# Kernel optimization log

Hardware: AMD Instinct MI355X
Metric: run time of the kernel (lower is better)

The kernel has to match this reference:

```python
import jax, jax.numpy as jnp
import numpy as np

MAX_FRAMES = 12
TOPK = 49
NUM_SAMPLES = 500
SIGMA = 0.05
EPS = 1e-5
NOISE_KEY = jax.random.key(1)


def _ln(x, g, b):
    m = x.mean(-1, keepdims=True)
    v = ((x - m) ** 2).mean(-1, keepdims=True)
    return (x - m) / jnp.sqrt(v + EPS) * g + b


def _gelu(x):
    return jax.nn.gelu(x, approximate=False)  # torch nn.GELU default is exact erf


def _predict(x, guid, ln_in_g, ln_in_b, W_in, ln_gd_g, ln_gd_b, W_gd, W_out1, W_out2):
    # x: (b, N, D), guid: (b, 1, D) -> score (b, N, 1)
    b, N, D = x.shape
    local = _gelu(_ln(x, ln_in_g, ln_in_b) @ W_in)            # (b, N, D/2)
    glob = _gelu(_ln(guid, ln_gd_g, ln_gd_b) @ W_gd)          # (b, 1, D/2); LN is per-token so repeat-then-LN == LN-then-broadcast
    glob = jnp.broadcast_to(glob, (b, N, glob.shape[-1]))
    h = jnp.concatenate([local, glob], axis=-1)               # (b, N, D)
    return jnp.tanh(_gelu(h @ W_out1) @ W_out2)               # (b, N, 1)


def _perturbed_topk(scores):
    # scores: (b, d) -> soft indicators (b, k, d); same math as one_hot(sorted topk idx).mean over samples,
    # computed by scatter-add instead of materializing the (b, ns, k, d) one-hot tensor.
    b, d = scores.shape
    noise = jax.random.normal(NOISE_KEY, (b, NUM_SAMPLES, d), scores.dtype)
    perturbed = scores[:, None, :] + SIGMA * noise            # (b, ns, d)
    _, idx = jax.lax.top_k(perturbed, TOPK)                   # (b, ns, k)
    idx = jnp.sort(idx, axis=-1)
    bi = jnp.arange(b)[:, None, None]
    ki = jnp.arange(TOPK)[None, None, :]
    ind = jnp.zeros((b, TOPK, d), scores.dtype).at[bi, ki, idx].add(1.0 / NUM_SAMPLES)
    return ind


def setup_inputs() -> dict:
    key = jax.random.key(0)
    ks = jax.random.split(key, 9)
    B, F, N, D = 8, MAX_FRAMES, 196, 512
    H = D // 2
    s = 0.02
    return {
        "x": jax.random.normal(ks[0], (B, F * N, D), jnp.float32),
        "guidance_frame": jax.random.normal(ks[1], (B, F, D), jnp.float32),
        "guidance_sentence": jax.random.normal(ks[2], (B, 1, D), jnp.float32),
        "ln_in_g": jnp.ones((D,), jnp.float32),
        "ln_in_b": jnp.zeros((D,), jnp.float32),
        "W_in": jax.random.normal(ks[3], (D, H), jnp.float32) * s,
        "ln_gd_g": jnp.ones((D,), jnp.float32),
        "ln_gd_b": jnp.zeros((D,), jnp.float32),
        "W_gd": jax.random.normal(ks[4], (D, H), jnp.float32) * s,
        "W_out1": jax.random.normal(ks[5], (D, H), jnp.float32) * s,
        "W_out2": jax.random.normal(ks[6], (H, 1), jnp.float32) * s,
    }


def reference(x, guidance_frame, guidance_sentence, ln_in_g, ln_in_b, W_in, ln_gd_g, ln_gd_b, W_gd, W_out1, W_out2):
    B, L, D = x.shape
    N = L // MAX_FRAMES
    xf = x.reshape(B * MAX_FRAMES, N, D)                       # (b', N, D)
    gf = guidance_frame.reshape(B * MAX_FRAMES, 1, D)
    gs = jnp.broadcast_to(guidance_sentence, (B, MAX_FRAMES, D)).reshape(B * MAX_FRAMES, 1, D)
    s1 = _predict(xf, gf, ln_in_g, ln_in_b, W_in, ln_gd_g, ln_gd_b, W_gd, W_out1, W_out2)[..., 0]
    s2 = _predict(xf, gs, ln_in_g, ln_in_b, W_in, ln_gd_g, ln_gd_b, W_gd, W_out1, W_out2)[..., 0]
    score = s1 + s2                                            # (b', N)
    ind = _perturbed_topk(score)                               # (b', k, N)
    selected = jnp.einsum('bkl,bld->bkd', ind, xf)             # (b', k, D)
    return selected.reshape(B, MAX_FRAMES, TOPK, D)
```

## Files before the change

kernel.cpp:

```cpp
#include <hip/hip_runtime.h>
#include <stdint.h>

#define DEV __device__ __forceinline__

#define BP 96
#define NTOK 196
#define DIM 512
#define HID 256
#define NS 500
#define TOPK 49
#define ROWS (BP * NTOK)
#define GBLK (ROWS / 32)
#define SPB 10
#define CNTSZ (TOPK * NTOK)

typedef _Float16 f16x8 __attribute__((ext_vector_type(8)));
typedef float f32x4 __attribute__((ext_vector_type(4)));

DEV float gelu32(float v) {
  return 0.5f * v * (1.0f + erff(v * 0.70710678f));
}

DEV void threefry2x32(uint32_t x0, uint32_t x1, uint32_t& o0, uint32_t& o1) {
  const uint32_t k0 = 0u, k1 = 1u;
  const uint32_t k2 = 0x1BD11BDAu ^ k0 ^ k1;
  x0 += k0; x1 += k1;
#define TF_R(r) { x0 += x1; x1 = (x1 << (r)) | (x1 >> (32 - (r))); x1 ^= x0; }
  TF_R(13) TF_R(15) TF_R(26) TF_R(6)
  x0 += k1; x1 += k2 + 1u;
  TF_R(17) TF_R(29) TF_R(16) TF_R(24)
  x0 += k2; x1 += k0 + 2u;
  TF_R(13) TF_R(15) TF_R(26) TF_R(6)
  x0 += k0; x1 += k1 + 3u;
  TF_R(17) TF_R(29) TF_R(16) TF_R(24)
  x0 += k1; x1 += k2 + 4u;
  TF_R(13) TF_R(15) TF_R(26) TF_R(6)
  x0 += k2; x1 += k0 + 5u;
#undef TF_R
  o0 = x0; o1 = x1;
}

DEV float erfinv_xla(float x) {
  float w = -__logf(fmaf(-x, x, 1.0f));
  float ws = w - 2.5f;
  float ps = 2.81022636e-08f;
  ps = fmaf(ps, ws, 3.43273939e-07f);
  ps = fmaf(ps, ws, -3.5233877e-06f);
  ps = fmaf(ps, ws, -4.39150654e-06f);
  ps = fmaf(ps, ws, 0.00021858087f);
  ps = fmaf(ps, ws, -0.00125372503f);
  ps = fmaf(ps, ws, -0.00417768164f);
  ps = fmaf(ps, ws, 0.246640727f);
  ps = fmaf(ps, ws, 1.50140941f);
  float r = ps;
  if (__ballot(w >= 5.0f) != 0ull) {
    float wl = sqrtf(w) - 3.0f;
    float pl = -0.000200214257f;
    pl = fmaf(pl, wl, 0.000100950558f);
    pl = fmaf(pl, wl, 0.00134934322f);
    pl = fmaf(pl, wl, -0.00367342844f);
    pl = fmaf(pl, wl, 0.00573950773f);
    pl = fmaf(pl, wl, -0.0076224613f);
    pl = fmaf(pl, wl, 0.00943887047f);
    pl = fmaf(pl, wl, 1.00167406f);
    pl = fmaf(pl, wl, 2.83297682f);
    r = (w < 5.0f) ? ps : pl;
  }
  return r * x;
}

DEV float noise_at(unsigned g) {
  unsigned o0, o1;
  threefry2x32(0u, g, o0, o1);
  unsigned bits = o0 ^ o1;
  float f = __uint_as_float((bits >> 9) | 0x3f800000u) - 1.0f;
  float u = f * 2.0f - 0.99999994f;
  u = fmaxf(-0.99999994f, u);
  return 1.41421356f * erfinv_xla(u);
}

DEV size_t pack_idx(int k, int col) {
  int t = k >> 5, kg = (k >> 3) & 3, e = k & 7;
  return (((size_t)(t * 4 + kg) * 256) + col) * 8 + e;
}

#define PRE_GLOB 192
#define PRE_PREP 512
#define PRE_STATS (ROWS / 4)
__global__ __launch_bounds__(256) void k_pre(
    const float* __restrict__ gf, const float* __restrict__ gs,
    const float* __restrict__ lng, const float* __restrict__ lnb,
    const float* __restrict__ Wgd, const float* __restrict__ Wout1,
    float* __restrict__ cout,
    const float* __restrict__ Win,
    const float* __restrict__ g_in, const float* __restrict__ b_in,
    _Float16* __restrict__ Pgh, _Float16* __restrict__ Pgl,
    _Float16* __restrict__ P1h, _Float16* __restrict__ P1l,
    float* __restrict__ gwv, float* __restrict__ bwv,
    const float* __restrict__ x, float* __restrict__ stats) {
  const int bid = blockIdx.x;
  if (bid < PRE_GLOB) {
    int bq = bid >> 1, which = bid & 1;
    const float* row = which ? (gs + (size_t)(bq / 12) * DIM) : (gf + (size_t)bq * DIM);
    __shared__ float lx[DIM];
    __shared__ float sg[HID];
    __shared__ double sred[8];
    int tid = threadIdx.x, lane = tid & 63, wv = tid >> 6;
    float v0 = row[tid], v1 = row[tid + 256];
    double s = (double)v0 + v1, q = (double)v0 * v0 + (double)v1 * v1;
    #pragma unroll
    for (int m = 1; m < 64; m <<= 1) { s += __shfl_xor(s, m); q += __shfl_xor(q, m); }
    if (lane == 0) { sred[wv * 2] = s; sred[wv * 2 + 1] = q; }
    __syncthreads();
    double ts = sred[0] + sred[2] + sred[4] + sred[6];
    double tq = sred[1] + sred[3] + sred[5] + sred[7];
    double mean = ts / 512.0;
    double var = tq / 512.0 - mean * mean;
    float mn = (float)mean;
    float rs = (float)(1.0 / sqrt(var + 1e-5));
    lx[tid]       = (v0 - mn) * rs * lng[tid] + lnb[tid];
    lx[tid + 256] = (v1 - mn) * rs * lng[tid + 256] + lnb[tid + 256];
    __syncthreads();
    float acc = 0.0f;
    for (int d = 0; d < DIM; ++d) acc = fmaf(lx[d], Wgd[(size_t)d * HID + tid], acc);
    sg[tid] = gelu32(acc);
    __syncthreads();
    float c = 0.0f;
    for (int j = 0; j < HID; ++j) c = fmaf(sg[j], Wout1[(size_t)(HID + j) * HID + tid], c);
    cout[((size_t)which * BP + bq) * HID + tid] = c;
  } else if (bid < PRE_GLOB + PRE_PREP) {
    int b2 = bid - PRE_GLOB;
    int n = b2 & 255, half = b2 >> 8;
    if (half == 0) {
      __shared__ float wred[8];
      int tid = threadIdx.x, lane = tid & 63, wv = tid >> 6;
      float sgv = 0.0f, sbv = 0.0f;
      #pragma unroll
      for (int kk = 0; kk < 2; ++kk) {
        int k = tid + kk * 256;
        float w = Win[(size_t)k * HID + n];
        float wg = w * g_in[k];
        _Float16 h = (_Float16)wg;
        size_t pi = pack_idx(k, n);
        Pgh[pi] = h;
        Pgl[pi] = (_Float16)(wg - (float)h);
        sgv += wg;
        sbv = fmaf(b_in[k], w, sbv);
      }
      #pragma unroll
      for (int m = 1; m < 64; m <<= 1) { sgv += __shfl_xor(sgv, m); sbv += __shfl_xor(sbv, m); }
      if (lane == 0) { wred[wv * 2] = sgv; wred[wv * 2 + 1] = sbv; }
      __syncthreads();
      if (tid == 0) {
        gwv[n] = wred[0] + wred[2] + wred[4] + wred[6];
        bwv[n] = wred[1] + wred[3] + wred[5] + wred[7];
      }
    } else {
      int k = threadIdx.x;
      float v = Wout1[(size_t)k * HID + n];
      _Float16 h = (_Float16)v;
      size_t pi = pack_idx(k, n);
      P1h[pi] = h;
      P1l[pi] = (_Float16)(v - (float)h);
    }
  } else {
    int r = (bid - PRE_GLOB - PRE_PREP) * 4 + (threadIdx.x >> 6);
    int lane = threadIdx.x & 63;
    const float4* xr = (const float4*)(x + (size_t)r * DIM);
    float4 a = xr[lane], c = xr[lane + 64];
    double s = (double)a.x + a.y + a.z + a.w + (double)c.x + c.y + c.z + c.w;
    double q = (double)a.x * a.x + (double)a.y * a.y + (double)a.z * a.z + (double)a.w * a.w +
               (double)c.x * c.x + (double)c.y * c.y + (double)c.z * c.z + (double)c.w * c.w;
    #pragma unroll
    for (int m = 1; m < 64; m <<= 1) { s += __shfl_xor(s, m); q += __shfl_xor(q, m); }
    if (lane == 0) {
      double mean = s / 512.0;
      double var = q / 512.0 - mean * mean;
      stats[r * 2]     = (float)mean;
      stats[r * 2 + 1] = (float)(1.0 / sqrt(var + 1e-5));
    }
  }
}

#define LOADA(src0, src1, t, pb)                                               \
  {                                                                            \
    axv[pb][0] = *(const float4*)((src0) + (t) * 32);                          \
    axv[pb][1] = *(const float4*)((src0) + (t) * 32 + 4);                      \
    axv[pb][2] = *(const float4*)((src1) + (t) * 32);                          \
    axv[pb][3] = *(const float4*)((src1) + (t) * 32 + 4);                      \
  }

#define LOADB(bh, bl, t, pb)                                                   \
  {                                                                            \
    _Pragma("unroll")                                                          \
    for (int ni = 0; ni < 4; ++ni) {                                           \
      bxh[pb][ni] = *(const f16x8*)((bh) + (size_t)(t) * 8192 + ni * 128);     \
      bxl[pb][ni] = *(const f16x8*)((bl) + (size_t)(t) * 8192 + ni * 128);     \
    }                                                                          \
  }

#define SPLITA(pb, fah, fal)                                                   \
  {                                                                            \
    _Pragma("unroll")                                                          \
    for (int mi = 0; mi < 2; ++mi) {                                           \
      float va[8];                                                             \
      *(float4*)&va[0] = axv[pb][mi * 2];                                      \
      *(float4*)&va[4] = axv[pb][mi * 2 + 1];                                  \
      _Pragma("unroll")                                                        \
      for (int e = 0; e < 8; ++e) {                                            \
        _Float16 h = (_Float16)va[e];                                          \
        fah[mi][e] = h;                                                        \
        fal[mi][e] = (_Float16)(va[e] - (float)h);                             \
      }                                                                        \
    }                                                                          \
  }

#define MFMA_CHUNK(pb, fah, fal)                                               \
  {                                                                            \
    _Pragma("unroll")                                                          \
    for (int mi = 0; mi < 2; ++mi)                                             \
      _Pragma("unroll")                                                        \
      for (int ni = 0; ni < 4; ++ni) {                                         \
        acc[mi][ni] = __builtin_amdgcn_mfma_f32_16x16x32_f16(fah[mi], bxh[pb][ni], acc[mi][ni], 0, 0, 0); \
        acc[mi][ni] = __builtin_amdgcn_mfma_f32_16x16x32_f16(fah[mi], bxl[pb][ni], acc[mi][ni], 0, 0, 0); \
        acc[mi][ni] = __builtin_amdgcn_mfma_f32_16x16x32_f16(fal[mi], bxh[pb][ni], acc[mi][ni], 0, 0, 0); \
      }                                                                        \
  }

__global__ __launch_bounds__(256) void k_g1(
    const float* __restrict__ x, const float* __restrict__ stats,
    const _Float16* __restrict__ Pgh, const _Float16* __restrict__ Pgl,
    const float* __restrict__ gwv, const float* __restrict__ bwv,
    float* __restrict__ local_) {
  __shared__ float stage[32 * HID];
  const int tid = threadIdx.x, lane = tid & 63, w = tid >> 6;
  const int kg = lane >> 4, lr = lane & 15;
  const int gr0 = blockIdx.x * 32;

  const float* asrc0 = x + (size_t)(gr0 + lr) * DIM + kg * 8;
  const float* asrc1 = x + (size_t)(gr0 + 16 + lr) * DIM + kg * 8;
  const _Float16* bh = Pgh + ((size_t)kg * 256 + w * 64 + lr) * 8;
  const _Float16* bl = Pgl + ((size_t)kg * 256 + w * 64 + lr) * 8;

  f32x4 acc[2][4];
  const f32x4 z4 = {0.f, 0.f, 0.f, 0.f};
  #pragma unroll
  for (int mi = 0; mi < 2; ++mi)
    #pragma unroll
    for (int ni = 0; ni < 4; ++ni) acc[mi][ni] = z4;
  float4 axv[2][4];
  f16x8 bxh[2][4], bxl[2][4];

  LOADA(asrc0, asrc1, 0, 0)
  LOADB(bh, bl, 0, 0)
  #pragma unroll
  for (int t = 0; t < 16; ++t) {
    const int pb = t & 1;
    if (t + 1 < 16) {
      LOADA(asrc0, asrc1, t + 1, pb ^ 1)
      LOADB(bh, bl, t + 1, pb ^ 1)
    }
    f16x8 fah[2], fal[2];
    SPLITA(pb, fah, fal)
    MFMA_CHUNK(pb, fah, fal)
  }

  float gwc[4], bwc[4];
  #pragma unroll
  for (int ni = 0; ni < 4; ++ni) {
    int col = w * 64 + ni * 16 + lr;
    gwc[ni] = gwv[col];
    bwc[ni] = bwv[col];
  }
  #pragma unroll
  for (int mi = 0; mi < 2; ++mi)
    #pragma unroll
    for (int i = 0; i < 4; ++i) {
      int rrel = mi * 16 + kg * 4 + i;
      int row = gr0 + rrel;
      float mn = stats[row * 2], rs = stats[row * 2 + 1];
      #pragma unroll
      for (int ni = 0; ni < 4; ++ni) {
        int col = w * 64 + ni * 16 + lr;
        float v = rs * acc[mi][ni][i] - rs * mn * gwc[ni] + bwc[ni];
        stage[rrel * HID + col] = gelu32(v);
      }
    }
  __syncthreads();
  {
    const float4* st4 = (const float4*)stage;
    float4* dst = (float4*)(local_ + (size_t)gr0 * HID);
    #pragma unroll
    for (int i = 0; i < 8; ++i) dst[tid + i * 256] = st4[tid + i * 256];
  }
}

__global__ __launch_bounds__(256) void k_g2(
    const float* __restrict__ local_,
    const _Float16* __restrict__ P1h, const _Float16* __restrict__ P1l,
    const float* __restrict__ W2, const float* __restrict__ c1,
    const float* __restrict__ c2, float* __restrict__ scores) {
  __shared__ float red1[32][4], red2[32][4];
  const int tid = threadIdx.x, lane = tid & 63, w = tid >> 6;
  const int kg = lane >> 4, lr = lane & 15;
  const int gr0 = blockIdx.x * 32;

  const float* asrc0 = local_ + (size_t)(gr0 + lr) * HID + kg * 8;
  const float* asrc1 = local_ + (size_t)(gr0 + 16 + lr) * HID + kg * 8;
  const _Float16* bh = P1h + ((size_t)kg * 256 + w * 64 + lr) * 8;
  const _Float16* bl = P1l + ((size_t)kg * 256 + w * 64 + lr) * 8;

  f32x4 acc[2][4];
  const f32x4 z4 = {0.f, 0.f, 0.f, 0.f};
  #pragma unroll
  for (int mi = 0; mi < 2; ++mi)
    #pragma unroll
    for (int ni = 0; ni < 4; ++ni) acc[mi][ni] = z4;
  float4 axv[2][4];
  f16x8 bxh[2][4], bxl[2][4];

  LOADA(asrc0, asrc1, 0, 0)
  LOADB(bh, bl, 0, 0)
  #pragma unroll
  for (int t = 0; t < 8; ++t) {
    const int pb = t & 1;
    if (t + 1 < 8) {
      LOADA(asrc0, asrc1, t + 1, pb ^ 1)
      LOADB(bh, bl, t + 1, pb ^ 1)
    }
    f16x8 fah[2], fal[2];
    SPLITA(pb, fah, fal)
    MFMA_CHUNK(pb, fah, fal)
  }

  float w2v[4];
  #pragma unroll
  for (int ni = 0; ni < 4; ++ni) w2v[ni] = W2[w * 64 + ni * 16 + lr];
  #pragma unroll
  for (int mi = 0; mi < 2; ++mi) {
    #pragma unroll
    for (int i = 0; i < 4; ++i) {
      int row = gr0 + mi * 16 + kg * 4 + i;
      int bf = row / NTOK;
      float p1 = 0.f, p2 = 0.f;
      #pragma unroll
      for (int ni = 0; ni < 4; ++ni) {
        int col = w * 64 + ni * 16 + lr;
        float u = acc[mi][ni][i];
        p1 = fmaf(gelu32(u + c1[(size_t)bf * HID + col]), w2v[ni], p1);
        p2 = fmaf(gelu32(u + c2[(size_t)bf * HID + col]), w2v[ni], p2);
      }
      #pragma unroll
      for (int m = 1; m < 16; m <<= 1) { p1 += __shfl_xor(p1, m); p2 += __shfl_xor(p2, m); }
      if (lr == 0) {
        red1[mi * 16 + kg * 4 + i][w] = p1;
        red2[mi * 16 + kg * 4 + i][w] = p2;
      }
    }
  }
  __syncthreads();
  if (tid < 32) {
    float s1 = red1[tid][0] + red1[tid][1] + red1[tid][2] + red1[tid][3];
    float s2 = red2[tid][0] + red2[tid][1] + red2[tid][2] + red2[tid][3];
    scores[gr0 + tid] = tanhf(s1) + tanhf(s2);
  }
}

__global__ __launch_bounds__(512) void k_topk(const float* __restrict__ scores,
                                              unsigned short* __restrict__ partial) {
  const int b = blockIdx.x, chunk = blockIdx.y;
  const int tid = threadIdx.x, lane = tid & 63, wv = tid >> 6;
  __shared__ float sc_s[NTOK];
  __shared__ int cnt_s[CNTSZ];
  if (tid < NTOK) sc_s[tid] = scores[b * NTOK + tid];
  for (int i = tid; i < CNTSZ; i += 512) cnt_s[i] = 0;

  const int s_first = chunk + SPB * wv;
  const unsigned gb = (unsigned)b * NS * 196u;

  float n_tail = 0.0f;
  {
    int si = lane >> 2, t = lane & 3;
    int s = s_first + si * (SPB * 8);
    if (lane < 28 && s < NS) {
      n_tail = noise_at(gb + (unsigned)s * 196u + 192u + (unsigned)t);
    }
  }
  __syncthreads();

  int si = 0;
  for (int s = s_first; s < NS; s += SPB * 8, ++si) {
    const unsigned gbase = gb + (unsigned)s * 196u;
    unsigned key[4];
    #pragma unroll
    for (int c = 0; c < 3; ++c) {
      float n = noise_at(gbase + (unsigned)(c * 64 + lane));
      float p = fmaf(0.05f, n, sc_s[c * 64 + lane]);
      unsigned ub = __float_as_uint(p);
      key[c] = (ub & 0x80000000u) ? ~ub : (ub | 0x80000000u);
    }
    {
      float n = __shfl(n_tail, si * 4 + (lane & 3));
      float p = fmaf(0.05f, n, sc_s[192 + (lane & 3)]);
      unsigned ub = __float_as_uint(p);
      unsigned k3 = (ub & 0x80000000u) ? ~ub : (ub | 0x80000000u);
      key[3] = (lane < 4) ? k3 : 0u;
    }
    unsigned prefix = 0u;
    bool exact = false;
    for (int bit = 31; bit >= 0; --bit) {
      unsigned t = prefix | (1u << bit);
      int cn = 0;
      #pragma unroll
      for (int c = 0; c < 4; ++c) cn += __popcll(__ballot(key[c] >= t));
      if (cn >= TOPK) {
        prefix = t;
        if (cn == TOPK) { exact = true; break; }
      }
    }
    unsigned long long lt = (1ull << lane) - 1ull;
    bool sel[4];
    if (exact) {
      #pragma unroll
      for (int c = 0; c < 4; ++c) sel[c] = key[c] >= prefix;
    } else {
      unsigned long long mE[4];
      int cntG = 0;
      #pragma unroll
      for (int c = 0; c < 4; ++c) {
        cntG += __popcll(__ballot(key[c] > prefix));
        mE[c] = __ballot(key[c] == prefix);
      }
      int need = TOPK - cntG;
      #pragma unroll
      for (int c = 0; c < 4; ++c) {
        int er = 0;
        for (int cc = 0; cc < c; ++cc) er += __popcll(mE[cc]);
        er += __popcll(mE[c] & lt);
        sel[c] = (key[c] > prefix) || ((key[c] == prefix) && (er < need));
      }
    }
    unsigned long long mS[4];
    #pragma unroll
    for (int c = 0; c < 4; ++c) mS[c] = __ballot(sel[c]);
    int base = 0;
    #pragma unroll
    for (int c = 0; c < 4; ++c) {
      if (sel[c]) {
        int rank = base + __popcll(mS[c] & lt);
        int j = c * 64 + lane;
        atomicAdd(&cnt_s[rank * NTOK + j], 1);
      }
      base += __popcll(mS[c]);
    }
  }
  __syncthreads();
  unsigned short* dst = partial + ((size_t)b * SPB + chunk) * CNTSZ;
  for (int i = tid; i < CNTSZ; i += 512) dst[i] = (unsigned short)cnt_s[i];
}

__global__ __launch_bounds__(256) void k_out(const float* __restrict__ x,
                                             const unsigned short* __restrict__ partial,
                                             float* __restrict__ out) {
  int bid = blockIdx.x;
  int b = bid % BP, k = bid / BP;
  __shared__ float swv[NTOK];
  __shared__ int idxs[NTOK];
  __shared__ int wcnt[4];
  __shared__ int wbase[5];
  __shared__ float4 part2[128];
  const int tid = threadIdx.x, lane = tid & 63, wv = tid >> 6;

  int cval = 0;
  if (tid < NTOK) {
    #pragma unroll
    for (int cc = 0; cc < SPB; ++cc)
      cval += partial[((size_t)b * SPB + cc) * CNTSZ + k * NTOK + tid];
  }
  unsigned long long m = __ballot(cval != 0);
  if (lane == 0) wcnt[wv] = __popcll(m);
  __syncthreads();
  if (tid == 0) {
    int a = 0;
    #pragma unroll
    for (int i = 0; i < 4; ++i) { wbase[i] = a; a += wcnt[i]; }
    wbase[4] = a;
  }
  __syncthreads();
  if (cval != 0) {
    int pos = wbase[wv] + __popcll(m & ((1ull << lane) - 1ull));
    idxs[pos] = tid;
    swv[pos] = (float)cval * 0.002f;
  }
  __syncthreads();
  const int n = wbase[4];
  const int half = tid >> 7, d4 = tid & 127;
  const int i0 = half ? (n + 1) / 2 : 0;
  const int i1 = half ? n : (n + 1) / 2;
  float a0 = 0, a1 = 0, a2 = 0, a3 = 0;
  for (int i = i0; i < i1; ++i) {
    float w = swv[i];
    float4 xv = *(const float4*)(x + ((size_t)(b * NTOK + idxs[i])) * DIM + d4 * 4);
    a0 = fmaf(w, xv.x, a0); a1 = fmaf(w, xv.y, a1);
    a2 = fmaf(w, xv.z, a2); a3 = fmaf(w, xv.w, a3);
  }
  if (half == 1) part2[d4] = make_float4(a0, a1, a2, a3);
  __syncthreads();
  if (half == 0) {
    float4 p = part2[d4];
    float4 o = make_float4(a0 + p.x, a1 + p.y, a2 + p.z, a3 + p.w);
    *(float4*)(out + ((size_t)(b * TOPK + k)) * DIM + d4 * 4) = o;
  }
}

extern "C" void kernel_launch(void* const* d_in, const int* in_sizes, int n_in,
                              void* d_out, int out_size, void* d_ws, size_t ws_size,
                              hipStream_t stream) {
  const float* x       = (const float*)d_in[0];
  const float* gf      = (const float*)d_in[1];
  const float* gs      = (const float*)d_in[2];
  const float* ln_in_g = (const float*)d_in[3];
  const float* ln_in_b = (const float*)d_in[4];
  const float* W_in    = (const float*)d_in[5];
  const float* ln_gd_g = (const float*)d_in[6];
  const float* ln_gd_b = (const float*)d_in[7];
  const float* W_gd    = (const float*)d_in[8];
  const float* W_out1  = (const float*)d_in[9];
  const float* W_out2  = (const float*)d_in[10];
  float* out = (float*)d_out;

  char* p = (char*)d_ws;
  float* local_  = (float*)p;             p += (size_t)ROWS * HID * 4;
  unsigned short* partial = (unsigned short*)p; p += (size_t)BP * SPB * CNTSZ * 2;
  float* stats   = (float*)p;             p += (size_t)ROWS * 2 * 4;
  float* c1      = (float*)p;             p += (size_t)BP * HID * 4;
  float* c2      = (float*)p;             p += (size_t)BP * HID * 4;
  float* scores  = (float*)p;             p += (size_t)ROWS * 4;
  _Float16* Pgh  = (_Float16*)p;          p += (size_t)HID * DIM * 2;
  _Float16* Pgl  = (_Float16*)p;          p += (size_t)HID * DIM * 2;
  _Float16* P1h  = (_Float16*)p;          p += (size_t)HID * HID * 2;
  _Float16* P1l  = (_Float16*)p;          p += (size_t)HID * HID * 2;
  float* gwv     = (float*)p;             p += HID * 4;
  float* bwv     = (float*)p;             p += HID * 4;

  k_pre<<<PRE_GLOB + PRE_PREP + PRE_STATS, 256, 0, stream>>>(
      gf, gs, ln_gd_g, ln_gd_b, W_gd, W_out1, c1,
      W_in, ln_in_g, ln_in_b, Pgh, Pgl, P1h, P1l, gwv, bwv, x, stats);
  k_g1<<<GBLK, 256, 0, stream>>>(x, stats, Pgh, Pgl, gwv, bwv, local_);
  k_g2<<<GBLK, 256, 0, stream>>>(local_, P1h, P1l, W_out2, c1, c2, scores);
  k_topk<<<dim3(BP, SPB), 512, 0, stream>>>(scores, partial);
  k_out<<<BP * TOPK, 256, 0, stream>>>(x, partial, out);
}
```

Baseline: 167.8 us.

## Fuse the two MLP GEMM kernels and keep GELU activations in LDS

Merges k_g1 and k_g2 into a single kernel. The 32x256 GELU activation tile stays in padded shared memory and feeds the second GEMM directly, instead of being written to a global buffer and read back. This removes one kernel launch and the global round trip of the intermediate activations. The padded LDS stage is slightly larger, which may lower occupancy and lengthen each block's serial work.

```diff
diff --git a/kernel.cpp b/kernel.cpp
--- a/kernel.cpp
+++ b/kernel.cpp
@@ -13,6 +13,7 @@
 #define GBLK (ROWS / 32)
 #define SPB 10
 #define CNTSZ (TOPK * NTOK)
+#define SPAD 260
 
 typedef _Float16 f16x8 __attribute__((ext_vector_type(8)));
 typedef float f32x4 __attribute__((ext_vector_type(4)));
@@ -190,6 +191,14 @@
     axv[pb][3] = *(const float4*)((src1) + (t) * 32 + 4);                      \
   }
 
+#define LOADA_LDS(t, pb)                                                       \
+  {                                                                            \
+    axv[pb][0] = *(const float4*)&stage[lr * SPAD + (t) * 32 + kg * 8];        \
+    axv[pb][1] = *(const float4*)&stage[lr * SPAD + (t) * 32 + kg * 8 + 4];    \
+    axv[pb][2] = *(const float4*)&stage[(16 + lr) * SPAD + (t) * 32 + kg * 8]; \
+    axv[pb][3] = *(const float4*)&stage[(16 + lr) * SPAD + (t) * 32 + kg * 8 + 4]; \
+  }
+
 #define LOADB(bh, bl, t, pb)                                                   \
   {                                                                            \
     _Pragma("unroll")                                                          \
@@ -227,12 +236,15 @@
       }                                                                        \
   }
 
-__global__ __launch_bounds__(256) void k_g1(
+__global__ __launch_bounds__(256) void k_gemm(
     const float* __restrict__ x, const float* __restrict__ stats,
     const _Float16* __restrict__ Pgh, const _Float16* __restrict__ Pgl,
     const float* __restrict__ gwv, const float* __restrict__ bwv,
-    float* __restrict__ local_) {
-  __shared__ float stage[32 * HID];
+    const _Float16* __restrict__ P1h, const _Float16* __restrict__ P1l,
+    const float* __restrict__ W2, const float* __restrict__ c1,
+    const float* __restrict__ c2, float* __restrict__ scores) {
+  __shared__ float stage[32 * SPAD];
+  __shared__ float red1[32][4], red2[32][4];
   const int tid = threadIdx.x, lane = tid & 63, w = tid >> 6;
   const int kg = lane >> 4, lr = lane & 15;
   const int gr0 = blockIdx.x * 32;
@@ -241,6 +253,8 @@
   const float* asrc1 = x + (size_t)(gr0 + 16 + lr) * DIM + kg * 8;
   const _Float16* bh = Pgh + ((size_t)kg * 256 + w * 64 + lr) * 8;
   const _Float16* bl = Pgl + ((size_t)kg * 256 + w * 64 + lr) * 8;
+  const _Float16* bh2 = P1h + ((size_t)kg * 256 + w * 64 + lr) * 8;
+  const _Float16* bl2 = P1l + ((size_t)kg * 256 + w * 64 + lr) * 8;
 
   f32x4 acc[2][4];
   const f32x4 z4 = {0.f, 0.f, 0.f, 0.f};
@@ -265,68 +279,43 @@
     MFMA_CHUNK(pb, fah, fal)
   }
 
-  float gwc[4], bwc[4];
-  #pragma unroll
-  for (int ni = 0; ni < 4; ++ni) {
-    int col = w * 64 + ni * 16 + lr;
-    gwc[ni] = gwv[col];
-    bwc[ni] = bwv[col];
-  }
+  {
+    float gwc[4], bwc[4];
+    #pragma unroll
+    for (int ni = 0; ni < 4; ++ni) {
+      int col = w * 64 + ni * 16 + lr;
+      gwc[ni] = gwv[col];
+      bwc[ni] = bwv[col];
+    }
+    #pragma unroll
+    for (int mi = 0; mi < 2; ++mi)
+      #pragma unroll
+      for (int i = 0; i < 4; ++i) {
+        int rrel = mi * 16 + kg * 4 + i;
+        int row = gr0 + rrel;
+        float mn = stats[row * 2], rs = stats[row * 2 + 1];
+        #pragma unroll
+        for (int ni = 0; ni < 4; ++ni) {
+          int col = w * 64 + ni * 16 + lr;
+          float v = rs * acc[mi][ni][i] - rs * mn * gwc[ni] + bwc[ni];
+          stage[rrel * SPAD + col] = gelu32(v);
+        }
+      }
+  }
+  LOADB(bh2, bl2, 0, 0)
+  __syncthreads();
+
   #pragma unroll
   for (int mi = 0; mi < 2; ++mi)
     #pragma unroll
-    for (int i = 0; i < 4; ++i) {
-      int rrel = mi * 16 + kg * 4 + i;
-      int row = gr0 + rrel;
-      float mn = stats[row * 2], rs = stats[row * 2 + 1];
-      #pragma unroll
-      for (int ni = 0; ni < 4; ++ni) {
-        int col = w * 64 + ni * 16 + lr;
-        float v = rs * acc[mi][ni][i] - rs * mn * gwc[ni] + bwc[ni];
-        stage[rrel * HID + col] = gelu32(v);
-      }
-    }
-  __syncthreads();
-  {
-    const float4* st4 = (const float4*)stage;
-    float4* dst = (float4*)(local_ + (size_t)gr0 * HID);
-    #pragma unroll
-    for (int i = 0; i < 8; ++i) dst[tid + i * 256] = st4[tid + i * 256];
-  }
-}
-
-__global__ __launch_bounds__(256) void k_g2(
-    const float* __restrict__ local_,
-    const _Float16* __restrict__ P1h, const _Float16* __restrict__ P1l,
-    const float* __restrict__ W2, const float* __restrict__ c1,
-    const float* __restrict__ c2, float* __restrict__ scores) {
-  __shared__ float red1[32][4], red2[32][4];
-  const int tid = threadIdx.x, lane = tid & 63, w = tid >> 6;
-  const int kg = lane >> 4, lr = lane & 15;
-  const int gr0 = blockIdx.x * 32;
-
-  const float* asrc0 = local_ + (size_t)(gr0 + lr) * HID + kg * 8;
-  const float* asrc1 = local_ + (size_t)(gr0 + 16 + lr) * HID + kg * 8;
-  const _Float16* bh = P1h + ((size_t)kg * 256 + w * 64 + lr) * 8;
-  const _Float16* bl = P1l + ((size_t)kg * 256 + w * 64 + lr) * 8;
-
-  f32x4 acc[2][4];
-  const f32x4 z4 = {0.f, 0.f, 0.f, 0.f};
-  #pragma unroll
-  for (int mi = 0; mi < 2; ++mi)
-    #pragma unroll
     for (int ni = 0; ni < 4; ++ni) acc[mi][ni] = z4;
-  float4 axv[2][4];
-  f16x8 bxh[2][4], bxl[2][4];
-
-  LOADA(asrc0, asrc1, 0, 0)
-  LOADB(bh, bl, 0, 0)
+  LOADA_LDS(0, 0)
   #pragma unroll
   for (int t = 0; t < 8; ++t) {
     const int pb = t & 1;
     if (t + 1 < 8) {
-      LOADA(asrc0, asrc1, t + 1, pb ^ 1)
-      LOADB(bh, bl, t + 1, pb ^ 1)
+      LOADA_LDS(t + 1, pb ^ 1)
+      LOADB(bh2, bl2, t + 1, pb ^ 1)
     }
     f16x8 fah[2], fal[2];
     SPLITA(pb, fah, fal)
@@ -530,7 +519,6 @@
   float* out = (float*)d_out;
 
   char* p = (char*)d_ws;
-  float* local_  = (float*)p;             p += (size_t)ROWS * HID * 4;
   unsigned short* partial = (unsigned short*)p; p += (size_t)BP * SPB * CNTSZ * 2;
   float* stats   = (float*)p;             p += (size_t)ROWS * 2 * 4;
   float* c1      = (float*)p;             p += (size_t)BP * HID * 4;
@@ -546,8 +534,8 @@
   k_pre<<<PRE_GLOB + PRE_PREP + PRE_STATS, 256, 0, stream>>>(
       gf, gs, ln_gd_g, ln_gd_b, W_gd, W_out1, c1,
       W_in, ln_in_g, ln_in_b, Pgh, Pgl, P1h, P1l, gwv, bwv, x, stats);
-  k_g1<<<GBLK, 256, 0, stream>>>(x, stats, Pgh, Pgl, gwv, bwv, local_);
-  k_g2<<<GBLK, 256, 0, stream>>>(local_, P1h, P1l, W_out2, c1, c2, scores);
+  k_gemm<<<GBLK, 256, 0, stream>>>(x, stats, Pgh, Pgl, gwv, bwv,
+                                   P1h, P1l, W_out2, c1, c2, scores);
   k_topk<<<dim3(BP, SPB), 512, 0, stream>>>(scores, partial);
   k_out<<<BP * TOPK, 256, 0, stream>>>(x, partial, out);
 }
```

Result: faster. 154.8 us (-7.7%).
